# Kernel optimization log

Measured on AMD Instinct MI355X. Metric: run time of the kernel, lower is better.

Reference implementation:

```python
import jax, jax.numpy as jnp
import numpy as np

NODE_DIM = 256
EDGE_DIM = 128
HEADS = 8
HEAD_DIM = 32
HIDDEN = HEADS * HEAD_DIM  # 256
B, N = 2, 768
LN_EPS = 1e-5


def _layernorm(x, w, b):
    mu = jnp.mean(x, axis=-1, keepdims=True)
    var = jnp.mean(jnp.square(x - mu), axis=-1, keepdims=True)
    return (x - mu) * jax.lax.rsqrt(var + LN_EPS) * w + b


def setup_inputs() -> dict:
    key = jax.random.key(0)
    ks = jax.random.split(key, 10)
    s_node = NODE_DIM ** -0.5
    s_edge = EDGE_DIM ** -0.5
    s_hid = HIDDEN ** -0.5
    return {
        "node": jax.random.normal(ks[0], (B, N, NODE_DIM), jnp.float32),
        "edge": jax.random.normal(ks[1], (B, N, N, EDGE_DIM), jnp.float32),
        "ln_node_w": jnp.ones((NODE_DIM,), jnp.float32),
        "ln_node_b": jnp.zeros((NODE_DIM,), jnp.float32),
        "ln_edge_w": jnp.ones((EDGE_DIM,), jnp.float32),
        "ln_edge_b": jnp.zeros((EDGE_DIM,), jnp.float32),
        "Wq": jax.random.normal(ks[2], (NODE_DIM, HIDDEN), jnp.float32) * s_node,
        "Wk": jax.random.normal(ks[3], (NODE_DIM, HIDDEN), jnp.float32) * s_node,
        "Wv": jax.random.normal(ks[4], (NODE_DIM, HIDDEN), jnp.float32) * s_node,
        "Wb": jax.random.normal(ks[5], (EDGE_DIM, HEADS), jnp.float32) * s_edge,
        "Wg": jax.random.normal(ks[6], (NODE_DIM, HIDDEN), jnp.float32) * s_node,
        "bg": jnp.zeros((HIDDEN,), jnp.float32),
        "Wo": jax.random.normal(ks[7], (HIDDEN, NODE_DIM), jnp.float32) * s_hid,
        "bo": jnp.zeros((NODE_DIM,), jnp.float32),
    }


def reference(node, edge, ln_node_w, ln_node_b, ln_edge_w, ln_edge_b,
              Wq, Wk, Wv, Wb, Wg, bg, Wo, bo):
    scale = HEAD_DIM ** -0.5
    x = _layernorm(node, ln_node_w, ln_node_b)          # [b, i, node_dim]
    y = _layernorm(edge, ln_edge_w, ln_edge_b)          # [b, i, j, edge_dim]

    def heads(t):  # [b, i, hidden] -> [b, h, i, d]
        b_, i_, _ = t.shape
        return t.reshape(b_, i_, HEADS, HEAD_DIM).transpose(0, 2, 1, 3)

    q = heads(x @ Wq)
    k = heads(x @ Wk)
    v = heads(x @ Wv)
    g = heads(jax.nn.sigmoid(x @ Wg + bg))
    bias = jnp.einsum('bije,eh->bhij', y, Wb)           # [b, h, i, j]

    logits = jnp.einsum('bhid,bhjd->bhij', q, k) * scale + bias
    attn = jax.nn.softmax(logits, axis=-1)
    res = jnp.einsum('bhij,bhjd->bhid', attn, v) * g    # gated values
    res = res.transpose(0, 2, 1, 3).reshape(node.shape[0], node.shape[1], HIDDEN)
    return res @ Wo + bo
```

## Files before the change

### kernel.cpp

```cpp
#include <hip/hip_runtime.h>
#include <hip/hip_bf16.h>
#include <math.h>

#define BN 1536
#define NN 768
#define SCALE 0.17677669529663687f
#define TJ 64

__global__ __launch_bounds__(256) void k_lnproj(
    const float* __restrict__ node, const float* __restrict__ lnw,
    const float* __restrict__ lnb, const float* __restrict__ Wq,
    const float* __restrict__ Wk, const float* __restrict__ Wv,
    const float* __restrict__ Wg, const float* __restrict__ bg,
    float* __restrict__ q, float* __restrict__ k,
    float* __restrict__ v, float* __restrict__ g)
{
    __shared__ float xs[8][256];
    const int tid = threadIdx.x;
    const int wave = tid >> 6, lane = tid & 63;
    const int row0 = blockIdx.x * 8;

    #pragma unroll
    for (int rr = 0; rr < 2; ++rr) {
        const int r = wave * 2 + rr;
        float4 xv = ((const float4*)node)[(size_t)(row0 + r) * 64 + lane];
        float s1 = xv.x + xv.y + xv.z + xv.w;
        float s2 = fmaf(xv.x, xv.x, fmaf(xv.y, xv.y, fmaf(xv.z, xv.z, xv.w * xv.w)));
        #pragma unroll
        for (int off = 32; off > 0; off >>= 1) {
            s1 += __shfl_xor(s1, off);
            s2 += __shfl_xor(s2, off);
        }
        const float mu = s1 * (1.f / 256.f);
        const float rstd = rsqrtf(s2 * (1.f / 256.f) - mu * mu + 1e-5f);
        float4 w4 = ((const float4*)lnw)[lane];
        float4 b4 = ((const float4*)lnb)[lane];
        xs[r][lane * 4 + 0] = (xv.x - mu) * rstd * w4.x + b4.x;
        xs[r][lane * 4 + 1] = (xv.y - mu) * rstd * w4.y + b4.y;
        xs[r][lane * 4 + 2] = (xv.z - mu) * rstd * w4.z + b4.z;
        xs[r][lane * 4 + 3] = (xv.w - mu) * rstd * w4.w + b4.w;
    }
    __syncthreads();

    float aq[8] = {}, ak[8] = {}, av[8] = {}, ag[8] = {};
    for (int e4 = 0; e4 < 64; ++e4) {
        const int e = e4 * 4;
        float wq_[4], wk_[4], wv_[4], wg_[4];
        #pragma unroll
        for (int t = 0; t < 4; ++t) {
            wq_[t] = Wq[(e + t) * 256 + tid];
            wk_[t] = Wk[(e + t) * 256 + tid];
            wv_[t] = Wv[(e + t) * 256 + tid];
            wg_[t] = Wg[(e + t) * 256 + tid];
        }
        #pragma unroll
        for (int r = 0; r < 8; ++r) {
            float4 xr = *(const float4*)&xs[r][e];
            aq[r] = fmaf(xr.x, wq_[0], fmaf(xr.y, wq_[1], fmaf(xr.z, wq_[2], fmaf(xr.w, wq_[3], aq[r]))));
            ak[r] = fmaf(xr.x, wk_[0], fmaf(xr.y, wk_[1], fmaf(xr.z, wk_[2], fmaf(xr.w, wk_[3], ak[r]))));
            av[r] = fmaf(xr.x, wv_[0], fmaf(xr.y, wv_[1], fmaf(xr.z, wv_[2], fmaf(xr.w, wv_[3], av[r]))));
            ag[r] = fmaf(xr.x, wg_[0], fmaf(xr.y, wg_[1], fmaf(xr.z, wg_[2], fmaf(xr.w, wg_[3], ag[r]))));
        }
    }
    const float bgv = bg[tid];
    #pragma unroll
    for (int r = 0; r < 8; ++r) {
        const size_t o = (size_t)(row0 + r) * 256 + tid;
        q[o] = aq[r];
        k[o] = ak[r];
        v[o] = av[r];
        g[o] = 1.f / (1.f + __expf(-(ag[r] + bgv)));
    }
}

__global__ __launch_bounds__(256) void k_attn(
    const float* __restrict__ edge,
    const float* __restrict__ lnw, const float* __restrict__ lnb,
    const float* __restrict__ Wb,
    const float* __restrict__ q, const float* __restrict__ k,
    const float* __restrict__ v, const float* __restrict__ g,
    float* __restrict__ res)
{
    __shared__ float bias_s[TJ][8];
    __shared__ float mrg[4][64][6];

    const int tid = threadIdx.x;
    const int wave = tid >> 6, lane = tid & 63;
    const int bi = blockIdx.x;
    const int b = bi / NN;
    const size_t ebase = (size_t)bi * NN * 128;

    const int sg = lane >> 4;
    const int gl = lane & 15;
    const float4 w0 = ((const float4*)lnw)[gl];
    const float4 w1 = ((const float4*)lnw)[16 + gl];
    const float4 b0 = ((const float4*)lnb)[gl];
    const float4 b1 = ((const float4*)lnb)[16 + gl];
    float wb[8][8];
    #pragma unroll
    for (int t = 0; t < 4; ++t) {
        float4 a0 = ((const float4*)Wb)[(gl * 4 + t) * 2];
        float4 a1 = ((const float4*)Wb)[(gl * 4 + t) * 2 + 1];
        wb[t][0] = a0.x; wb[t][1] = a0.y; wb[t][2] = a0.z; wb[t][3] = a0.w;
        wb[t][4] = a1.x; wb[t][5] = a1.y; wb[t][6] = a1.z; wb[t][7] = a1.w;
        float4 c0 = ((const float4*)Wb)[(64 + gl * 4 + t) * 2];
        float4 c1 = ((const float4*)Wb)[(64 + gl * 4 + t) * 2 + 1];
        wb[4 + t][0] = c0.x; wb[4 + t][1] = c0.y; wb[4 + t][2] = c0.z; wb[4 + t][3] = c0.w;
        wb[4 + t][4] = c1.x; wb[4 + t][5] = c1.y; wb[4 + t][6] = c1.z; wb[4 + t][7] = c1.w;
    }

    const float4 q4 = ((const float4*)q)[(size_t)bi * 64 + lane];
    float m = -3e38f, s = 0.f;
    float4 acc = make_float4(0.f, 0.f, 0.f, 0.f);
    const int h = lane >> 3;

    for (int jt = 0; jt < NN; jt += TJ) {
        #pragma unroll
        for (int pass = 0; pass < 4; ++pass) {
            const int ri = pass * 16 + wave * 4 + sg;
            const float* er = edge + ebase + (size_t)(jt + ri) * 128;
            const float4 e0 = ((const float4*)er)[gl];
            const float4 e1 = ((const float4*)er)[16 + gl];
            float s1 = e0.x + e0.y + e0.z + e0.w + e1.x + e1.y + e1.z + e1.w;
            float s2 = fmaf(e0.x, e0.x, fmaf(e0.y, e0.y, fmaf(e0.z, e0.z, e0.w * e0.w)));
            s2 = fmaf(e1.x, e1.x, fmaf(e1.y, e1.y, fmaf(e1.z, e1.z, fmaf(e1.w, e1.w, s2))));
            #pragma unroll
            for (int off = 8; off > 0; off >>= 1) {
                s1 += __shfl_xor(s1, off);
                s2 += __shfl_xor(s2, off);
            }
            const float mu = s1 * (1.f / 128.f);
            const float rstd = rsqrtf(s2 * (1.f / 128.f) - mu * mu + 1e-5f);
            float y[8];
            y[0] = (e0.x - mu) * rstd * w0.x + b0.x;
            y[1] = (e0.y - mu) * rstd * w0.y + b0.y;
            y[2] = (e0.z - mu) * rstd * w0.z + b0.z;
            y[3] = (e0.w - mu) * rstd * w0.w + b0.w;
            y[4] = (e1.x - mu) * rstd * w1.x + b1.x;
            y[5] = (e1.y - mu) * rstd * w1.y + b1.y;
            y[6] = (e1.z - mu) * rstd * w1.z + b1.z;
            y[7] = (e1.w - mu) * rstd * w1.w + b1.w;
            float p[8];
            #pragma unroll
            for (int hh = 0; hh < 8; ++hh) {
                float t = y[0] * wb[0][hh];
                #pragma unroll
                for (int e = 1; e < 8; ++e) t = fmaf(y[e], wb[e][hh], t);
                p[hh] = t;
            }
            #pragma unroll
            for (int off = 8; off > 0; off >>= 1) {
                #pragma unroll
                for (int hh = 0; hh < 8; ++hh) p[hh] += __shfl_xor(p[hh], off);
            }
            if (gl < 8) bias_s[ri][gl] = p[gl];
        }
        __syncthreads();

        for (int jj = wave; jj < TJ; jj += 4) {
            const int j = jt + jj;
            const float bias = bias_s[jj][h];
            const size_t kvbase = (size_t)(b * NN + j) * 64;
            const float4 kv = ((const float4*)k)[kvbase + lane];
            float dot = fmaf(q4.x, kv.x, fmaf(q4.y, kv.y, fmaf(q4.z, kv.z, q4.w * kv.w)));
            dot += __shfl_xor(dot, 1);
            dot += __shfl_xor(dot, 2);
            dot += __shfl_xor(dot, 4);
            const float logit = fmaf(dot, SCALE, bias);
            const float mn = fmaxf(m, logit);
            const float sc = __expf(m - mn);
            const float pj = __expf(logit - mn);
            s = fmaf(s, sc, pj);
            m = mn;
            const float4 vv = ((const float4*)v)[kvbase + lane];
            acc.x = fmaf(pj, vv.x, acc.x * sc);
            acc.y = fmaf(pj, vv.y, acc.y * sc);
            acc.z = fmaf(pj, vv.z, acc.z * sc);
            acc.w = fmaf(pj, vv.w, acc.w * sc);
        }
        __syncthreads();
    }

    mrg[wave][lane][0] = m;
    mrg[wave][lane][1] = s;
    mrg[wave][lane][2] = acc.x;
    mrg[wave][lane][3] = acc.y;
    mrg[wave][lane][4] = acc.z;
    mrg[wave][lane][5] = acc.w;
    __syncthreads();
    if (wave == 0) {
        float M = mrg[0][lane][0];
        #pragma unroll
        for (int w2 = 1; w2 < 4; ++w2) M = fmaxf(M, mrg[w2][lane][0]);
        float S = 0.f;
        float4 A = make_float4(0.f, 0.f, 0.f, 0.f);
        #pragma unroll
        for (int w2 = 0; w2 < 4; ++w2) {
            const float sc = __expf(mrg[w2][lane][0] - M);
            S = fmaf(mrg[w2][lane][1], sc, S);
            A.x = fmaf(mrg[w2][lane][2], sc, A.x);
            A.y = fmaf(mrg[w2][lane][3], sc, A.y);
            A.z = fmaf(mrg[w2][lane][4], sc, A.z);
            A.w = fmaf(mrg[w2][lane][5], sc, A.w);
        }
        const float4 g4 = ((const float4*)g)[(size_t)bi * 64 + lane];
        const float inv = 1.f / S;
        float4 r;
        r.x = A.x * inv * g4.x;
        r.y = A.y * inv * g4.y;
        r.z = A.z * inv * g4.z;
        r.w = A.w * inv * g4.w;
        ((float4*)res)[(size_t)bi * 64 + lane] = r;
    }
}

__global__ __launch_bounds__(256) void k_outproj(
    const float* __restrict__ res, const float* __restrict__ Wo,
    const float* __restrict__ bo, float* __restrict__ out)
{
    __shared__ float xs[8][256];
    const int tid = threadIdx.x;
    const int row0 = blockIdx.x * 8;

    #pragma unroll
    for (int t = tid; t < 512; t += 256)
        ((float4*)&xs[0][0])[t] = ((const float4*)(res + (size_t)row0 * 256))[t];
    __syncthreads();

    float a[8] = {};
    for (int e4 = 0; e4 < 64; ++e4) {
        const int e = e4 * 4;
        float w_[4];
        #pragma unroll
        for (int t = 0; t < 4; ++t) w_[t] = Wo[(e + t) * 256 + tid];
        #pragma unroll
        for (int r = 0; r < 8; ++r) {
            float4 xr = *(const float4*)&xs[r][e];
            a[r] = fmaf(xr.x, w_[0], fmaf(xr.y, w_[1], fmaf(xr.z, w_[2], fmaf(xr.w, w_[3], a[r]))));
        }
    }
    const float bov = bo[tid];
    #pragma unroll
    for (int r = 0; r < 8; ++r)
        out[(size_t)(row0 + r) * 256 + tid] = a[r] + bov;
}

extern "C" void kernel_launch(void* const* d_in, const int* in_sizes, int n_in,
                              void* d_out, int out_size, void* d_ws, size_t ws_size,
                              hipStream_t stream) {
    const float* node = (const float*)d_in[0];
    const float* edge = (const float*)d_in[1];
    const float* lnnw = (const float*)d_in[2];
    const float* lnnb = (const float*)d_in[3];
    const float* lnew = (const float*)d_in[4];
    const float* lneb = (const float*)d_in[5];
    const float* Wq   = (const float*)d_in[6];
    const float* Wk   = (const float*)d_in[7];
    const float* Wv   = (const float*)d_in[8];
    const float* Wb   = (const float*)d_in[9];
    const float* Wg   = (const float*)d_in[10];
    const float* bg   = (const float*)d_in[11];
    const float* Wo   = (const float*)d_in[12];
    const float* bo   = (const float*)d_in[13];
    float* out = (float*)d_out;

    float* ws = (float*)d_ws;
    const size_t NT = (size_t)BN * 256;
    float* q   = ws;
    float* k   = ws + NT;
    float* v   = ws + 2 * NT;
    float* g   = ws + 3 * NT;
    float* res = ws + 4 * NT;

    k_lnproj<<<BN / 8, 256, 0, stream>>>(node, lnnw, lnnb, Wq, Wk, Wv, Wg, bg, q, k, v, g);
    k_attn<<<BN, 256, 0, stream>>>(edge, lnew, lneb, Wb, q, k, v, g, res);
    k_outproj<<<BN / 8, 256, 0, stream>>>(res, Wo, bo, out);
}
```

Baseline: 411.4 us.

## Split edge-bias into separate streaming kernel with folded LayerNorm algebra

Moves the edge LayerNorm plus bias projection out of the attention kernel into a grid-stride streaming kernel. That kernel folds the LN weight into Wb and computes bias = rstd*(e·W' - mu*sum W') + b·Wb, so it needs one pass and one reduction round. The attention kernel then reads a precomputed bias buffer, processes two keys per iteration, and drops the per-tile syncthreads. The query scale is folded into q at projection time. This adds a round-trip of a 1536x768x8 bias buffer through global memory in exchange for a better-overlapped streaming read of the large edge tensor.

Result: no change. 405.3 us (-1.5%).

```diff
diff --git a/kernel.cpp b/kernel.cpp
--- a/kernel.cpp
+++ b/kernel.cpp
@@ -5,7 +5,14 @@
 #define BN 1536
 #define NN 768
 #define SCALE 0.17677669529663687f
-#define TJ 64
+#define NROWS (BN * NN)
+
+__device__ __forceinline__ float sel8(const float* a, int idx) {
+    float r = a[0];
+#pragma unroll
+    for (int t = 1; t < 8; ++t) r = (idx == t) ? a[t] : r;
+    return r;
+}
 
 __global__ __launch_bounds__(256) void k_lnproj(
     const float* __restrict__ node, const float* __restrict__ lnw,
@@ -20,13 +27,13 @@
     const int wave = tid >> 6, lane = tid & 63;
     const int row0 = blockIdx.x * 8;
 
-    #pragma unroll
+#pragma unroll
     for (int rr = 0; rr < 2; ++rr) {
         const int r = wave * 2 + rr;
         float4 xv = ((const float4*)node)[(size_t)(row0 + r) * 64 + lane];
         float s1 = xv.x + xv.y + xv.z + xv.w;
         float s2 = fmaf(xv.x, xv.x, fmaf(xv.y, xv.y, fmaf(xv.z, xv.z, xv.w * xv.w)));
-        #pragma unroll
+#pragma unroll
         for (int off = 32; off > 0; off >>= 1) {
             s1 += __shfl_xor(s1, off);
             s2 += __shfl_xor(s2, off);
@@ -46,14 +53,14 @@
     for (int e4 = 0; e4 < 64; ++e4) {
         const int e = e4 * 4;
         float wq_[4], wk_[4], wv_[4], wg_[4];
-        #pragma unroll
+#pragma unroll
         for (int t = 0; t < 4; ++t) {
             wq_[t] = Wq[(e + t) * 256 + tid];
             wk_[t] = Wk[(e + t) * 256 + tid];
             wv_[t] = Wv[(e + t) * 256 + tid];
             wg_[t] = Wg[(e + t) * 256 + tid];
         }
-        #pragma unroll
+#pragma unroll
         for (int r = 0; r < 8; ++r) {
             float4 xr = *(const float4*)&xs[r][e];
             aq[r] = fmaf(xr.x, wq_[0], fmaf(xr.y, wq_[1], fmaf(xr.z, wq_[2], fmaf(xr.w, wq_[3], aq[r]))));
@@ -63,122 +70,134 @@
         }
     }
     const float bgv = bg[tid];
-    #pragma unroll
+#pragma unroll
     for (int r = 0; r < 8; ++r) {
         const size_t o = (size_t)(row0 + r) * 256 + tid;
-        q[o] = aq[r];
+        q[o] = aq[r] * SCALE;
         k[o] = ak[r];
         v[o] = av[r];
         g[o] = 1.f / (1.f + __expf(-(ag[r] + bgv)));
     }
 }
 
-__global__ __launch_bounds__(256) void k_attn(
-    const float* __restrict__ edge,
-    const float* __restrict__ lnw, const float* __restrict__ lnb,
-    const float* __restrict__ Wb,
+__global__ __launch_bounds__(256) void k_bias(
+    const float* __restrict__ edge, const float* __restrict__ lnw,
+    const float* __restrict__ lnb, const float* __restrict__ Wb,
+    float* __restrict__ bias)
+{
+    const int tid = threadIdx.x;
+    const int gl = tid & 15;
+
+    float wbf[8][8];
+    float c1p[8], c0p[8];
+#pragma unroll
+    for (int hh = 0; hh < 8; ++hh) { c1p[hh] = 0.f; c0p[hh] = 0.f; }
+#pragma unroll
+    for (int t = 0; t < 8; ++t) {
+        const int c = gl * 8 + t;
+        const float w = lnw[c], bb = lnb[c];
+#pragma unroll
+        for (int hh = 0; hh < 8; ++hh) {
+            const float wb_ = Wb[c * 8 + hh];
+            wbf[t][hh] = w * wb_;
+            c1p[hh] += wbf[t][hh];
+            c0p[hh] = fmaf(bb, wb_, c0p[hh]);
+        }
+    }
+#pragma unroll
+    for (int off = 1; off < 16; off <<= 1) {
+#pragma unroll
+        for (int hh = 0; hh < 8; ++hh) {
+            c1p[hh] += __shfl_xor(c1p[hh], off);
+            c0p[hh] += __shfl_xor(c0p[hh], off);
+        }
+    }
+    const float c1s = sel8(c1p, gl & 7);
+    const float c0s = sel8(c0p, gl & 7);
+
+    const int stride = gridDim.x * 16;
+    for (int r = blockIdx.x * 16 + (tid >> 4); r < NROWS; r += stride) {
+        const float4 e0 = ((const float4*)edge)[(size_t)r * 32 + gl * 2];
+        const float4 e1 = ((const float4*)edge)[(size_t)r * 32 + gl * 2 + 1];
+        float s1 = (e0.x + e0.y) + (e0.z + e0.w) + ((e1.x + e1.y) + (e1.z + e1.w));
+        float s2 = fmaf(e0.x, e0.x, fmaf(e0.y, e0.y, fmaf(e0.z, e0.z, e0.w * e0.w)));
+        s2 = fmaf(e1.x, e1.x, fmaf(e1.y, e1.y, fmaf(e1.z, e1.z, fmaf(e1.w, e1.w, s2))));
+        float d[8];
+#pragma unroll
+        for (int hh = 0; hh < 8; ++hh) {
+            float t0 = e0.x * wbf[0][hh];
+            t0 = fmaf(e0.y, wbf[1][hh], t0);
+            t0 = fmaf(e0.z, wbf[2][hh], t0);
+            t0 = fmaf(e0.w, wbf[3][hh], t0);
+            t0 = fmaf(e1.x, wbf[4][hh], t0);
+            t0 = fmaf(e1.y, wbf[5][hh], t0);
+            t0 = fmaf(e1.z, wbf[6][hh], t0);
+            t0 = fmaf(e1.w, wbf[7][hh], t0);
+            d[hh] = t0;
+        }
+#pragma unroll
+        for (int off = 1; off < 16; off <<= 1) {
+            s1 += __shfl_xor(s1, off);
+            s2 += __shfl_xor(s2, off);
+#pragma unroll
+            for (int hh = 0; hh < 8; ++hh) d[hh] += __shfl_xor(d[hh], off);
+        }
+        if (gl < 8) {
+            const float mu = s1 * (1.f / 128.f);
+            const float rstd = rsqrtf(s2 * (1.f / 128.f) - mu * mu + 1e-5f);
+            const float dh = sel8(d, gl);
+            bias[(size_t)r * 8 + gl] = rstd * (dh - mu * c1s) + c0s;
+        }
+    }
+}
+
+__global__ __launch_bounds__(256) void k_attn2(
+    const float* __restrict__ bias,
     const float* __restrict__ q, const float* __restrict__ k,
     const float* __restrict__ v, const float* __restrict__ g,
     float* __restrict__ res)
 {
-    __shared__ float bias_s[TJ][8];
     __shared__ float mrg[4][64][6];
-
     const int tid = threadIdx.x;
     const int wave = tid >> 6, lane = tid & 63;
     const int bi = blockIdx.x;
     const int b = bi / NN;
-    const size_t ebase = (size_t)bi * NN * 128;
-
-    const int sg = lane >> 4;
-    const int gl = lane & 15;
-    const float4 w0 = ((const float4*)lnw)[gl];
-    const float4 w1 = ((const float4*)lnw)[16 + gl];
-    const float4 b0 = ((const float4*)lnb)[gl];
-    const float4 b1 = ((const float4*)lnb)[16 + gl];
-    float wb[8][8];
-    #pragma unroll
-    for (int t = 0; t < 4; ++t) {
-        float4 a0 = ((const float4*)Wb)[(gl * 4 + t) * 2];
-        float4 a1 = ((const float4*)Wb)[(gl * 4 + t) * 2 + 1];
-        wb[t][0] = a0.x; wb[t][1] = a0.y; wb[t][2] = a0.z; wb[t][3] = a0.w;
-        wb[t][4] = a1.x; wb[t][5] = a1.y; wb[t][6] = a1.z; wb[t][7] = a1.w;
-        float4 c0 = ((const float4*)Wb)[(64 + gl * 4 + t) * 2];
-        float4 c1 = ((const float4*)Wb)[(64 + gl * 4 + t) * 2 + 1];
-        wb[4 + t][0] = c0.x; wb[4 + t][1] = c0.y; wb[4 + t][2] = c0.z; wb[4 + t][3] = c0.w;
-        wb[4 + t][4] = c1.x; wb[4 + t][5] = c1.y; wb[4 + t][6] = c1.z; wb[4 + t][7] = c1.w;
-    }
+    const int h = lane >> 3;
 
     const float4 q4 = ((const float4*)q)[(size_t)bi * 64 + lane];
+    const float* brow = bias + (size_t)bi * NN * 8;
+    const size_t kb = (size_t)b * NN * 64;
+
     float m = -3e38f, s = 0.f;
     float4 acc = make_float4(0.f, 0.f, 0.f, 0.f);
-    const int h = lane >> 3;
-
-    for (int jt = 0; jt < NN; jt += TJ) {
-        #pragma unroll
-        for (int pass = 0; pass < 4; ++pass) {
-            const int ri = pass * 16 + wave * 4 + sg;
-            const float* er = edge + ebase + (size_t)(jt + ri) * 128;
-            const float4 e0 = ((const float4*)er)[gl];
-            const float4 e1 = ((const float4*)er)[16 + gl];
-            float s1 = e0.x + e0.y + e0.z + e0.w + e1.x + e1.y + e1.z + e1.w;
-            float s2 = fmaf(e0.x, e0.x, fmaf(e0.y, e0.y, fmaf(e0.z, e0.z, e0.w * e0.w)));
-            s2 = fmaf(e1.x, e1.x, fmaf(e1.y, e1.y, fmaf(e1.z, e1.z, fmaf(e1.w, e1.w, s2))));
-            #pragma unroll
-            for (int off = 8; off > 0; off >>= 1) {
-                s1 += __shfl_xor(s1, off);
-                s2 += __shfl_xor(s2, off);
-            }
-            const float mu = s1 * (1.f / 128.f);
-            const float rstd = rsqrtf(s2 * (1.f / 128.f) - mu * mu + 1e-5f);
-            float y[8];
-            y[0] = (e0.x - mu) * rstd * w0.x + b0.x;
-            y[1] = (e0.y - mu) * rstd * w0.y + b0.y;
-            y[2] = (e0.z - mu) * rstd * w0.z + b0.z;
-            y[3] = (e0.w - mu) * rstd * w0.w + b0.w;
-            y[4] = (e1.x - mu) * rstd * w1.x + b1.x;
-            y[5] = (e1.y - mu) * rstd * w1.y + b1.y;
-            y[6] = (e1.z - mu) * rstd * w1.z + b1.z;
-            y[7] = (e1.w - mu) * rstd * w1.w + b1.w;
-            float p[8];
-            #pragma unroll
-            for (int hh = 0; hh < 8; ++hh) {
-                float t = y[0] * wb[0][hh];
-                #pragma unroll
-                for (int e = 1; e < 8; ++e) t = fmaf(y[e], wb[e][hh], t);
-                p[hh] = t;
-            }
-            #pragma unroll
-            for (int off = 8; off > 0; off >>= 1) {
-                #pragma unroll
-                for (int hh = 0; hh < 8; ++hh) p[hh] += __shfl_xor(p[hh], off);
-            }
-            if (gl < 8) bias_s[ri][gl] = p[gl];
-        }
-        __syncthreads();
-
-        for (int jj = wave; jj < TJ; jj += 4) {
-            const int j = jt + jj;
-            const float bias = bias_s[jj][h];
-            const size_t kvbase = (size_t)(b * NN + j) * 64;
-            const float4 kv = ((const float4*)k)[kvbase + lane];
-            float dot = fmaf(q4.x, kv.x, fmaf(q4.y, kv.y, fmaf(q4.z, kv.z, q4.w * kv.w)));
-            dot += __shfl_xor(dot, 1);
-            dot += __shfl_xor(dot, 2);
-            dot += __shfl_xor(dot, 4);
-            const float logit = fmaf(dot, SCALE, bias);
-            const float mn = fmaxf(m, logit);
-            const float sc = __expf(m - mn);
-            const float pj = __expf(logit - mn);
-            s = fmaf(s, sc, pj);
-            m = mn;
-            const float4 vv = ((const float4*)v)[kvbase + lane];
-            acc.x = fmaf(pj, vv.x, acc.x * sc);
-            acc.y = fmaf(pj, vv.y, acc.y * sc);
-            acc.z = fmaf(pj, vv.z, acc.z * sc);
-            acc.w = fmaf(pj, vv.w, acc.w * sc);
-        }
-        __syncthreads();
+
+    for (int jp = wave * 2; jp < NN; jp += 8) {
+        const int j0 = jp, j1 = jp + 1;
+        const float4 k0 = ((const float4*)k)[kb + (size_t)j0 * 64 + lane];
+        const float4 k1 = ((const float4*)k)[kb + (size_t)j1 * 64 + lane];
+        const float b0 = brow[j0 * 8 + h];
+        const float b1 = brow[j1 * 8 + h];
+        const float4 v0 = ((const float4*)v)[kb + (size_t)j0 * 64 + lane];
+        const float4 v1 = ((const float4*)v)[kb + (size_t)j1 * 64 + lane];
+
+        float d0 = fmaf(q4.x, k0.x, fmaf(q4.y, k0.y, fmaf(q4.z, k0.z, q4.w * k0.w)));
+        float d1 = fmaf(q4.x, k1.x, fmaf(q4.y, k1.y, fmaf(q4.z, k1.z, q4.w * k1.w)));
+        d0 += __shfl_xor(d0, 1); d1 += __shfl_xor(d1, 1);
+        d0 += __shfl_xor(d0, 2); d1 += __shfl_xor(d1, 2);
+        d0 += __shfl_xor(d0, 4); d1 += __shfl_xor(d1, 4);
+        const float l0 = d0 + b0;
+        const float l1 = d1 + b1;
+
+        const float mn = fmaxf(m, fmaxf(l0, l1));
+        const float sc = __expf(m - mn);
+        const float p0 = __expf(l0 - mn);
+        const float p1 = __expf(l1 - mn);
+        s = fmaf(s, sc, p0 + p1);
+        m = mn;
+        acc.x = fmaf(p1, v1.x, fmaf(p0, v0.x, acc.x * sc));
+        acc.y = fmaf(p1, v1.y, fmaf(p0, v0.y, acc.y * sc));
+        acc.z = fmaf(p1, v1.z, fmaf(p0, v0.z, acc.z * sc));
+        acc.w = fmaf(p1, v1.w, fmaf(p0, v0.w, acc.w * sc));
     }
 
     mrg[wave][lane][0] = m;
@@ -190,11 +209,11 @@
     __syncthreads();
     if (wave == 0) {
         float M = mrg[0][lane][0];
-        #pragma unroll
+#pragma unroll
         for (int w2 = 1; w2 < 4; ++w2) M = fmaxf(M, mrg[w2][lane][0]);
         float S = 0.f;
         float4 A = make_float4(0.f, 0.f, 0.f, 0.f);
-        #pragma unroll
+#pragma unroll
         for (int w2 = 0; w2 < 4; ++w2) {
             const float sc = __expf(mrg[w2][lane][0] - M);
             S = fmaf(mrg[w2][lane][1], sc, S);
@@ -222,7 +241,7 @@
     const int tid = threadIdx.x;
     const int row0 = blockIdx.x * 8;
 
-    #pragma unroll
+#pragma unroll
     for (int t = tid; t < 512; t += 256)
         ((float4*)&xs[0][0])[t] = ((const float4*)(res + (size_t)row0 * 256))[t];
     __syncthreads();
@@ -231,16 +250,16 @@
     for (int e4 = 0; e4 < 64; ++e4) {
         const int e = e4 * 4;
         float w_[4];
-        #pragma unroll
+#pragma unroll
         for (int t = 0; t < 4; ++t) w_[t] = Wo[(e + t) * 256 + tid];
-        #pragma unroll
+#pragma unroll
         for (int r = 0; r < 8; ++r) {
             float4 xr = *(const float4*)&xs[r][e];
             a[r] = fmaf(xr.x, w_[0], fmaf(xr.y, w_[1], fmaf(xr.z, w_[2], fmaf(xr.w, w_[3], a[r]))));
         }
     }
     const float bov = bo[tid];
-    #pragma unroll
+#pragma unroll
     for (int r = 0; r < 8; ++r)
         out[(size_t)(row0 + r) * 256 + tid] = a[r] + bov;
 }
@@ -266,13 +285,15 @@
 
     float* ws = (float*)d_ws;
     const size_t NT = (size_t)BN * 256;
-    float* q   = ws;
-    float* k   = ws + NT;
-    float* v   = ws + 2 * NT;
-    float* g   = ws + 3 * NT;
-    float* res = ws + 4 * NT;
+    float* q    = ws;
+    float* k    = ws + NT;
+    float* v    = ws + 2 * NT;
+    float* g    = ws + 3 * NT;
+    float* res  = ws + 4 * NT;
+    float* bias = ws + 5 * NT;
 
     k_lnproj<<<BN / 8, 256, 0, stream>>>(node, lnnw, lnnb, Wq, Wk, Wv, Wg, bg, q, k, v, g);
-    k_attn<<<BN, 256, 0, stream>>>(edge, lnew, lneb, Wb, q, k, v, g, res);
+    k_bias<<<2048, 256, 0, stream>>>(edge, lnew, lneb, Wb, bias);
+    k_attn2<<<BN, 256, 0, stream>>>(bias, q, k, v, g, res);
     k_outproj<<<BN / 8, 256, 0, stream>>>(res, Wo, bo, out);
 }
```
